# Kernel optimization log

Measured on AMD Instinct MI355X. Metric: run time of the kernel, lower is better.

## Reference

```python
import jax, jax.numpy as jnp
import numpy as np

B, T, C, H = 2, 4096, 512, 8
D = C // H          # head_size = 64
FF = 4 * C          # 2048
EPS = 1e-5


def _layernorm(x, g, b):
    mu = jnp.mean(x, axis=-1, keepdims=True)
    var = jnp.mean(jnp.square(x - mu), axis=-1, keepdims=True)
    return (x - mu) * jax.lax.rsqrt(var + EPS) * g + b


def setup_inputs() -> dict:
    key = jax.random.key(0)
    ks = jax.random.split(key, 10)
    s = 0.02
    return {
        "x":  jax.random.normal(ks[0], (B, T, C), dtype=jnp.float32),
        # per-head K/Q/V linears (bias=False) packed as [C, C] = concat over heads
        "Wq": jax.random.normal(ks[1], (C, C), dtype=jnp.float32) * s,
        "Wk": jax.random.normal(ks[2], (C, C), dtype=jnp.float32) * s,
        "Wv": jax.random.normal(ks[3], (C, C), dtype=jnp.float32) * s,
        "Wo": jax.random.normal(ks[4], (C, C), dtype=jnp.float32) * s,
        "bo": jnp.zeros((C,), dtype=jnp.float32),
        "W1": jax.random.normal(ks[5], (C, FF), dtype=jnp.float32) * s,
        "b1": jnp.zeros((FF,), dtype=jnp.float32),
        "W2": jax.random.normal(ks[6], (FF, C), dtype=jnp.float32) * s,
        "b2": jnp.zeros((C,), dtype=jnp.float32),
        "g1": jnp.ones((C,), dtype=jnp.float32),
        "be1": jnp.zeros((C,), dtype=jnp.float32),
        "g2": jnp.ones((C,), dtype=jnp.float32),
        "be2": jnp.zeros((C,), dtype=jnp.float32),
    }


def reference(x, Wq, Wk, Wv, Wo, bo, W1, b1, W2, b2, g1, be1, g2, be2):
    # --- self-attention on ln1(x), residual add ---
    h = _layernorm(x, g1, be1)                              # [B,T,C]
    q = (h @ Wq).reshape(B, T, H, D)
    k = (h @ Wk).reshape(B, T, H, D)
    v = (h @ Wv).reshape(B, T, H, D)
    # NOTE: original scales by C**-0.5 (n_embd), NOT head_size**-0.5
    scores = jnp.einsum("bthd,bshd->bhts", q, k) * (C ** -0.5)  # [B,H,T,T]
    causal = jnp.tril(jnp.ones((T, T), dtype=bool))
    scores = jnp.where(causal, scores, -jnp.inf)
    wei = jax.nn.softmax(scores, axis=-1)                   # dropout = identity (eval)
    attn = jnp.einsum("bhts,bshd->bthd", wei, v).reshape(B, T, C)
    x = x + (attn @ Wo + bo)                                # proj dropout = identity
    # --- feed-forward on ln2(x), residual add ---
    h2 = _layernorm(x, g2, be2)
    ff = jax.nn.relu(h2 @ W1 + b1) @ W2 + b2                # dropout = identity
    return x + ff
```

## Files before the change

### kernel.cpp

```cpp
#include <hip/hip_runtime.h>

typedef __attribute__((ext_vector_type(8))) __bf16 bf16x8;
typedef __attribute__((ext_vector_type(4))) __bf16 bf16x4;
typedef __attribute__((ext_vector_type(4))) float f32x4;
typedef __attribute__((ext_vector_type(4))) unsigned int u32x4;
typedef __attribute__((ext_vector_type(4))) unsigned short u16x4;
typedef __attribute__((ext_vector_type(8))) unsigned short u16x8;
typedef __attribute__((ext_vector_type(4))) short s16x4;
typedef unsigned short u16;

static __device__ __forceinline__ u16 f2b(float f) {
    unsigned u = __builtin_bit_cast(unsigned, f);
    u = (u + 0x7FFFu + ((u >> 16) & 1u)) >> 16;
    return (u16)u;
}
static __device__ __forceinline__ float b2f(u16 u) {
    return __builtin_bit_cast(float, ((unsigned)u) << 16);
}
static __device__ __forceinline__ float fexp2(float x) {
#if __has_builtin(__builtin_amdgcn_exp2f)
    return __builtin_amdgcn_exp2f(x);
#else
    return exp2f(x);
#endif
}
static __device__ __forceinline__ f32x4 mfma16(bf16x4 a, bf16x4 b, f32x4 c) {
#if __has_builtin(__builtin_amdgcn_mfma_f32_16x16x16_bf16)
    return __builtin_amdgcn_mfma_f32_16x16x16_bf16(a, b, c, 0, 0, 0);
#else
    return __builtin_amdgcn_mfma_f32_16x16x16bf16_1k(
        __builtin_bit_cast(s16x4, a), __builtin_bit_cast(s16x4, b), c, 0, 0, 0);
#endif
}

static __device__ __forceinline__ void gload16(const u16* g, u16* l) {
    __builtin_amdgcn_global_load_lds(
        (const __attribute__((address_space(1))) unsigned int*)g,
        (__attribute__((address_space(3))) unsigned int*)l, 16, 0, 0);
}

__global__ __launch_bounds__(256) void prep_w(
    const float* __restrict__ Wq, const float* __restrict__ Wk,
    const float* __restrict__ Wv, const float* __restrict__ Wo,
    const float* __restrict__ W1, const float* __restrict__ W2,
    u16* __restrict__ WqkvT, u16* __restrict__ WoT,
    u16* __restrict__ W1T, u16* __restrict__ W2T)
{
    const int i = blockIdx.x;
    const float* src; u16* dst; int K, N, nt, kt;
    if (i < 1024) {
        const int z = i >> 8, idx = i & 255;
        K = 512; N = 512; nt = (idx & 15) * 32; kt = (idx >> 4) * 32;
        if (z == 0)      { src = Wq; dst = WqkvT; }
        else if (z == 1) { src = Wk; dst = WqkvT + 512*512; }
        else if (z == 2) { src = Wv; dst = WqkvT + 1024*512; }
        else             { src = Wo; dst = WoT; }
    } else if (i < 2048) {
        const int idx = i - 1024;
        src = W1; dst = W1T; K = 512; N = 2048;
        nt = (idx & 63) * 32; kt = (idx >> 6) * 32;
    } else {
        const int idx = i - 2048;
        src = W2; dst = W2T; K = 2048; N = 512;
        nt = (idx & 15) * 32; kt = (idx >> 4) * 32;
    }
    __shared__ float tile[32][33];
    const int tx = threadIdx.x & 31, ty = threadIdx.x >> 5;
    #pragma unroll
    for (int r = 0; r < 4; ++r)
        tile[ty + r*8][tx] = src[(size_t)(kt + ty + r*8) * N + nt + tx];
    __syncthreads();
    #pragma unroll
    for (int r = 0; r < 4; ++r)
        dst[(size_t)(nt + ty + r*8) * K + kt + tx] = f2b(tile[tx][ty + r*8]);
}

__global__ __launch_bounds__(256) void ln_rows(
    const float* __restrict__ x, const float* __restrict__ g,
    const float* __restrict__ b, u16* __restrict__ out)
{
    const int row = blockIdx.x * 4 + (threadIdx.x >> 6);
    const int lane = threadIdx.x & 63;
    const float* xr = x + (size_t)row * 512;
    f32x4 v0 = *(const f32x4*)(xr + lane * 4);
    f32x4 v1 = *(const f32x4*)(xr + 256 + lane * 4);
    float s = v0[0]+v0[1]+v0[2]+v0[3]+v1[0]+v1[1]+v1[2]+v1[3];
    #pragma unroll
    for (int o = 1; o < 64; o <<= 1) s += __shfl_xor(s, o);
    const float mu = s * (1.0f / 512.0f);
    float s2 = 0.f;
    #pragma unroll
    for (int i = 0; i < 4; ++i) { float d0 = v0[i]-mu, d1 = v1[i]-mu; s2 += d0*d0 + d1*d1; }
    #pragma unroll
    for (int o = 1; o < 64; o <<= 1) s2 += __shfl_xor(s2, o);
    const float inv = rsqrtf(s2 * (1.0f/512.0f) + 1e-5f);
    f32x4 g0 = *(const f32x4*)(g + lane*4), g1 = *(const f32x4*)(g + 256 + lane*4);
    f32x4 b0 = *(const f32x4*)(b + lane*4), b1 = *(const f32x4*)(b + 256 + lane*4);
    u16x4 p0, p1;
    #pragma unroll
    for (int i = 0; i < 4; ++i) {
        p0[i] = f2b((v0[i]-mu)*inv*g0[i] + b0[i]);
        p1[i] = f2b((v1[i]-mu)*inv*g1[i] + b1[i]);
    }
    u16* orow = out + (size_t)row * 512;
    *(u16x4*)(orow + lane*4)       = p0;
    *(u16x4*)(orow + 256 + lane*4) = p1;
}

template<int FLAGS, int NB, int GX>
__global__ __launch_bounds__(256) void gemm_bt(
    const u16* __restrict__ A, const u16* __restrict__ BT,
    const int N, const int K,
    const float* __restrict__ bias, const float* __restrict__ res,
    void* __restrict__ outv, u16* __restrict__ vt)
{
    constexpr int RING = (NB == 2) ? 3 : 4;
    __shared__ __attribute__((aligned(16))) u16 As[RING * 4096];
    __shared__ __attribute__((aligned(16))) u16 Bs[RING * 2048 * NB];
    const int fid = blockIdx.x;
    const int xcd = fid & 7, s8 = fid >> 3;
    const int colb = s8 % GX, rl = s8 / GX;
    const int m0 = (xcd*8 + rl) << 7;
    const int n0 = colb * (64 * NB);
    const int tid = threadIdx.x, lane = tid & 63, w = tid >> 6;
    const int wr2 = w >> 1, wc = w & 1;
    const int g = lane >> 4, c = lane & 15;
    const f32x4 fz = {0.f, 0.f, 0.f, 0.f};

    f32x4 acc[4][2 * NB];
    #pragma unroll
    for (int m = 0; m < 4; ++m)
      #pragma unroll
      for (int n = 0; n < 2 * NB; ++n) acc[m][n] = fz;

    const int srow = tid >> 2;
    const int scs = (((tid & 3) ^ (srow & 3)) * 8);
    const u16* Ag = A  + (size_t)(m0 + srow)*K + scs;
    const u16* Bg = BT + (size_t)(n0 + srow)*K + scs;
    const size_t rstep = (size_t)64 * K;

    const int nkt = K >> 5;
    auto stage = [&](int slot, int kt) {
        const int k0 = kt << 5;
        u16* ad = &As[0] + slot*4096 + w*512;
        gload16(Ag + k0,         ad);
        gload16(Ag + rstep + k0, ad + 2048);
        u16* bd = &Bs[0] + slot*2048*NB + w*512;
        gload16(Bg + k0, bd);
        if constexpr (NB == 2) gload16(Bg + rstep + k0, bd + 2048);
    };
    stage(0, 0);
    stage(1, (1 < nkt) ? 1 : 0);
    if constexpr (RING == 4) stage(2, (2 < nkt) ? 2 : 0);

    for (int kt = 0; kt < nkt; ++kt) {
        if constexpr (NB == 2) asm volatile("s_waitcnt vmcnt(4)" ::: "memory");
        else                   asm volatile("s_waitcnt vmcnt(6)" ::: "memory");
        __builtin_amdgcn_s_barrier();
        asm volatile("" ::: "memory");
        {
            int tp = kt + RING - 1; if (tp >= nkt) tp = nkt - 1;
            int sl = kt + RING - 1; sl -= (sl / RING) * RING;
            stage(sl, tp);
        }
        const int rd = kt - (kt / RING) * RING;
        const u16* Ab = &As[0] + rd*4096;
        const u16* Bb = &Bs[0] + rd*2048*NB;
        bf16x8 af[4], bfr[2 * NB];
        #pragma unroll
        for (int m = 0; m < 4; ++m) {
            const int row = wr2*64 + m*16 + c;
            af[m] = *(const bf16x8*)(Ab + row*32 + (((g*16) ^ ((row&3)<<4)) >> 1));
        }
        #pragma unroll
        for (int n = 0; n < 2 * NB; ++n) {
            const int row = wc*(32*NB) + n*16 + c;
            bfr[n] = *(const bf16x8*)(Bb + row*32 + (((g*16) ^ ((row&3)<<4)) >> 1));
        }
        #pragma unroll
        for (int m = 0; m < 4; ++m)
          #pragma unroll
          for (int n = 0; n < 2 * NB; ++n)
            acc[m][n] = __builtin_amdgcn_mfma_f32_16x16x32_bf16(af[m], bfr[n], acc[m][n], 0, 0, 0);
    }

    #pragma unroll
    for (int m = 0; m < 4; ++m) {
        const int row = m0 + wr2*64 + m*16 + 4*g;
        #pragma unroll
        for (int n = 0; n < 2 * NB; ++n) {
            const int col = n0 + wc*(32*NB) + n*16 + c;
            const float bv = (FLAGS & 1) ? bias[col] : 0.0f;
            float vv[4];
            #pragma unroll
            for (int r = 0; r < 4; ++r) {
                float v = acc[m][n][r] + bv;
                if (FLAGS & 16) v *= (col < 512) ? 0.0637587246f : 1.0f;
                if (FLAGS & 2) v += res[(size_t)(row + r)*N + col];
                if (FLAGS & 4) v = fmaxf(v, 0.0f);
                vv[r] = v;
            }
            if ((FLAGS & 32) && col >= 1024) {
                u16x4 pv;
                #pragma unroll
                for (int r = 0; r < 4; ++r) pv[r] = f2b(vv[r]);
                *(u16x4*)(vt + (size_t)((row >> 12)*512 + (col - 1024))*4096
                             + (row & 4095)) = pv;
            } else if (FLAGS & 8) {
                #pragma unroll
                for (int r = 0; r < 4; ++r)
                    ((float*)outv)[(size_t)(row + r)*N + col] = vv[r];
            } else {
                #pragma unroll
                for (int r = 0; r < 4; ++r)
                    ((u16*)outv)[(size_t)(row + r)*N + col] = f2b(vv[r]);
            }
        }
    }
}

template<int FLAGS, int GX>
__global__ __launch_bounds__(256) void gemm_m64(
    const u16* __restrict__ A, const u16* __restrict__ BT,
    const int N, const int K,
    const float* __restrict__ bias, const float* __restrict__ res,
    void* __restrict__ outv)
{
    __shared__ __attribute__((aligned(16))) u16 As[4 * 2048];
    __shared__ __attribute__((aligned(16))) u16 Bs[4 * 2048];
    const int fid = blockIdx.x;
    const int xcd = fid & 7, s8 = fid >> 3;
    const int colb = s8 % GX, rl = s8 / GX;
    const int m0 = (xcd*16 + rl) << 6;
    const int n0 = colb << 6;
    const int tid = threadIdx.x, lane = tid & 63, w = tid >> 6;
    const int g = lane >> 4, c = lane & 15;
    const f32x4 fz = {0.f, 0.f, 0.f, 0.f};

    f32x4 acc[4] = {fz, fz, fz, fz};

    const int srow = tid >> 2;
    const int scs = (((tid & 3) ^ (srow & 3)) * 8);
    const u16* Ag = A  + (size_t)(m0 + srow)*K + scs;
    const u16* Bg = BT + (size_t)(n0 + srow)*K + scs;

    const int nkt = K >> 5;
    auto stage = [&](int slot, int kt) {
        const int k0 = kt << 5;
        gload16(Ag + k0, &As[0] + slot*2048 + w*512);
        gload16(Bg + k0, &Bs[0] + slot*2048 + w*512);
    };
    stage(0, 0);
    stage(1, (1 < nkt) ? 1 : 0);
    stage(2, (2 < nkt) ? 2 : 0);

    const int arow = w*16 + c;
    const int aoff = arow*32 + ((g ^ (arow & 3)) * 8);
    for (int kt = 0; kt < nkt; ++kt) {
        asm volatile("s_waitcnt vmcnt(4)" ::: "memory");
        __builtin_amdgcn_s_barrier();
        asm volatile("" ::: "memory");
        {
            int tp = kt + 3; if (tp >= nkt) tp = nkt - 1;
            stage((kt + 3) & 3, tp);
        }
        const int rd = kt & 3;
        const u16* Ab = &As[0] + rd*2048;
        const u16* Bb = &Bs[0] + rd*2048;
        const bf16x8 af = *(const bf16x8*)(Ab + aoff);
        bf16x8 bfr[4];
        #pragma unroll
        for (int n = 0; n < 4; ++n) {
            const int row = n*16 + c;
            bfr[n] = *(const bf16x8*)(Bb + row*32 + ((g ^ (row & 3)) * 8));
        }
        #pragma unroll
        for (int n = 0; n < 4; ++n)
            acc[n] = __builtin_amdgcn_mfma_f32_16x16x32_bf16(af, bfr[n], acc[n], 0, 0, 0);
    }

    const int row = m0 + w*16 + 4*g;
    #pragma unroll
    for (int n = 0; n < 4; ++n) {
        const int col = n0 + n*16 + c;
        const float bv = (FLAGS & 1) ? bias[col] : 0.0f;
        #pragma unroll
        for (int r = 0; r < 4; ++r) {
            float v = acc[n][r] + bv;
            if (FLAGS & 2) v += res[(size_t)(row + r)*N + col];
            if (FLAGS & 4) v = fmaxf(v, 0.0f);
            if (FLAGS & 8) ((float*)outv)[(size_t)(row + r)*N + col] = v;
            else           ((u16*)outv)[(size_t)(row + r)*N + col] = f2b(v);
        }
    }
}

__global__ __launch_bounds__(256, 3) void attn_fwd(
    const u16* __restrict__ qkv, const u16* __restrict__ vT,
    u16* __restrict__ part, u16* __restrict__ att)
{
    const int fid = blockIdx.x + 160 * blockIdx.y;
    const int xcd = fid & 7, s0i = fid >> 3;
    const int half = (s0i >= 160) ? 1 : 0;
    const int bh = xcd*2 + half, b = bh >> 3, h = bh & 7;
    const int i = 159 - (s0i - half*160);
    int qt, cch, nch;
    if (i < 16)      { qt = i;                         cch = 0;          nch = 1; }
    else if (i < 48) { int j = i-16; qt = 16 + (j>>1); cch = j & 1;      nch = 2; }
    else if (i < 96) { int j = i-48; int d3 = j/3; qt = 32 + d3; cch = j - 3*d3; nch = 3; }
    else             { int j = i-96; qt = 48 + (j>>2); cch = j & 3;      nch = 4; }
    const int ntl = qt + 1;
    const int t0 = (cch * ntl) / nch;
    const int t1 = ((cch + 1) * ntl) / nch;
    const int single = (nch == 1);

    const int tid = threadIdx.x, lane = tid & 63, w = tid >> 6;
    const int g = lane >> 4, c16 = lane & 15;
    __shared__ __attribute__((aligned(16))) u16 smem[20480];
    u16* Wb = smem + w*5120;
    float* lbuf = (float*)smem + 5120;

    const u16* qp  = qkv + (size_t)b*4096*1536 + h*64;
    const u16* kp  = qp + 512;
    const u16* vtp = vT + (size_t)bh*64*4096;

    const u16* kgA = kp + (size_t)(16*w + (lane>>3))*1536
                        + (((lane&7) ^ ((lane>>3)&7)) * 8);
    const u16* kgB = kgA + (size_t)8*1536;
    const int sd = lane >> 1;
    const u16* vgA = vtp + (size_t)sd*4096 + 16*w + (((lane&1) ^ ((sd>>2)&1)) * 8);
    const u16* vgB = vgA + (size_t)32*4096;

    const int kOff0 = c16*64 + ((g ^ (c16&7)) * 8);
    const int kOff1 = c16*64 + (((4+g) ^ (c16&7)) * 8);
    const int vroff = c16*16 + (((g>>1) ^ ((c16>>2)&1)) * 8) + (g&1)*4;

    const int Q0 = qt*64;
    bf16x8 qB[4][2];
    #pragma unroll
    for (int sub = 0; sub < 4; ++sub) {
        const u16* qr = qp + (size_t)(Q0 + sub*16 + c16)*1536 + g*8;
        qB[sub][0] = *(const bf16x8*)(qr);
        qB[sub][1] = *(const bf16x8*)(qr + 32);
    }

    const f32x4 fz = {0.f,0.f,0.f,0.f};
    f32x4 oacc[4][4];
    #pragma unroll
    for (int dt = 0; dt < 4; ++dt)
      #pragma unroll
      for (int sub = 0; sub < 4; ++sub) oacc[dt][sub] = fz;
    float lsum[4] = {0.f, 0.f, 0.f, 0.f};

    {
        const int kv0 = t0 << 6;
        u16* vd = Wb + 3072 + (t0 & 1)*1024;
        gload16(vgA + kv0, vd); gload16(vgB + kv0, vd + 512);
        u16* kd = Wb + (t0 % 3)*1024;
        const size_t ko0 = (size_t)kv0 * 1536;
        gload16(kgA + ko0, kd); gload16(kgB + ko0, kd + 512);
        const int tp1 = (t0+1 < t1) ? (t0+1) : (t1-1);
        u16* kd1 = Wb + ((t0+1) % 3)*1024;
        const size_t ko1 = (size_t)(tp1 << 6)*1536;
        gload16(kgA + ko1, kd1); gload16(kgB + ko1, kd1 + 512);
    }
    int krd = t0 % 3;
    int kwr = krd + 2; if (kwr >= 3) kwr -= 3;

    for (int t = t0; t < t1; ++t) {
        {
            const int tpv = (t+1 < t1) ? (t+1) : (t1-1);
            u16* vd = Wb + 3072 + ((t+1) & 1)*1024;
            gload16(vgA + (tpv << 6), vd); gload16(vgB + (tpv << 6), vd + 512);
            const int tpk = (t+2 < t1) ? (t+2) : (t1-1);
            u16* kd = Wb + kwr*1024;
            const size_t ko = (size_t)(tpk << 6)*1536;
            gload16(kgA + ko, kd); gload16(kgB + ko, kd + 512);
        }
        asm volatile("s_waitcnt vmcnt(6)" ::: "memory");
        const u16* Kb  = Wb + krd*1024;
        const u16* Vbp = Wb + 3072 + (t & 1)*1024;
        const bf16x8 kc0 = *(const bf16x8*)(Kb + kOff0);
        const bf16x8 kc1 = *(const bf16x8*)(Kb + kOff1);
        bf16x4 va[4];
        #pragma unroll
        for (int dt = 0; dt < 4; ++dt)
            va[dt] = *(const bf16x4*)(Vbp + dt*256 + vroff);
        f32x4 s[4];
        #pragma unroll
        for (int sub = 0; sub < 4; ++sub) {
            f32x4 sv = __builtin_amdgcn_mfma_f32_16x16x32_bf16(kc0, qB[sub][0], fz, 0, 0, 0);
            s[sub]   = __builtin_amdgcn_mfma_f32_16x16x32_bf16(kc1, qB[sub][1], sv, 0, 0, 0);
        }
        bf16x4 pt[4];
        if (t < qt) {
            #pragma unroll
            for (int sub = 0; sub < 4; ++sub) {
                float p0 = fexp2(s[sub][0]), p1 = fexp2(s[sub][1]);
                float p2 = fexp2(s[sub][2]), p3 = fexp2(s[sub][3]);
                lsum[sub] += (p0 + p1) + (p2 + p3);
                bf16x4 pv;
                pv[0] = (__bf16)p0; pv[1] = (__bf16)p1;
                pv[2] = (__bf16)p2; pv[3] = (__bf16)p3;
                pt[sub] = pv;
            }
        } else {
            const int kvbase = t*64 + 16*w + 4*g;
            #pragma unroll
            for (int sub = 0; sub < 4; ++sub) {
                const int qi = Q0 + sub*16 + c16;
                bf16x4 pv; float a = 0.f;
                #pragma unroll
                for (int r = 0; r < 4; ++r) {
                    float p = (kvbase + r <= qi) ? fexp2(s[sub][r]) : 0.0f;
                    a += p; pv[r] = (__bf16)p;
                }
                lsum[sub] += a; pt[sub] = pv;
            }
        }
        #pragma unroll
        for (int dt = 0; dt < 4; ++dt)
          #pragma unroll
          for (int sub = 0; sub < 4; ++sub)
            oacc[dt][sub] = mfma16(va[dt], pt[sub], oacc[dt][sub]);
        krd = (krd == 2) ? 0 : krd + 1;
        kwr = (kwr == 2) ? 0 : kwr + 1;
    }

    #pragma unroll
    for (int sub = 0; sub < 4; ++sub) {
        float v = lsum[sub];
        v += __shfl_xor(v, 16);
        v += __shfl_xor(v, 32);
        lsum[sub] = v;
    }

    asm volatile("s_waitcnt vmcnt(0)" ::: "memory");
    __syncthreads();
    #pragma unroll
    for (int sub = 0; sub < 4; ++sub)
        if (g == 0) lbuf[w*64 + sub*16 + c16] = lsum[sub];

    float* img = (float*)smem;
    f32x4 ofin[4];
    float ltot[4];
    #pragma unroll
    for (int dt = 0; dt < 4; ++dt) {
        #pragma unroll
        for (int sub = 0; sub < 4; ++sub)
            *(f32x4*)(img + w*1280 + (sub*16 + c16)*20 + g*4) = oacc[dt][sub];
        __syncthreads();
        if (dt == 0) {
            #pragma unroll
            for (int sub = 0; sub < 4; ++sub) {
                const int qr = sub*16 + c16;
                ltot[sub] = lbuf[qr] + lbuf[64 + qr] + lbuf[128 + qr] + lbuf[192 + qr];
            }
        }
        if (w == dt) {
            #pragma unroll
            for (int sub = 0; sub < 4; ++sub) {
                const int off = (sub*16 + c16)*20 + g*4;
                f32x4 a0 = *(const f32x4*)(img + off);
                f32x4 a1 = *(const f32x4*)(img + 1280 + off);
                f32x4 a2 = *(const f32x4*)(img + 2560 + off);
                f32x4 a3 = *(const f32x4*)(img + 3840 + off);
                ofin[sub] = (a0 + a1) + (a2 + a3);
            }
        }
        __syncthreads();
    }

    const int dbase = 16*w + 4*g;
    if (single) {
        #pragma unroll
        for (int sub = 0; sub < 4; ++sub) {
            const int qrow = sub*16 + c16;
            const float inv = 1.0f / ltot[sub];
            const f32x4 o = ofin[sub];
            u16x4 ov;
            ov[0] = f2b(o[0]*inv); ov[1] = f2b(o[1]*inv);
            ov[2] = f2b(o[2]*inv); ov[3] = f2b(o[3]*inv);
            *(u16x4*)(att + (size_t)(b*4096 + Q0 + qrow)*512 + h*64 + dbase) = ov;
        }
    } else {
        u16* onum = part + (size_t)(bh*160 + i) * 4224;
        float* lout = (float*)(onum + 4096);
        #pragma unroll
        for (int sub = 0; sub < 4; ++sub) {
            const int qrow = sub*16 + c16;
            const f32x4 o = ofin[sub];
            u16x4 ov;
            ov[0] = f2b(o[0]); ov[1] = f2b(o[1]);
            ov[2] = f2b(o[2]); ov[3] = f2b(o[3]);
            *(u16x4*)(onum + qrow*64 + dbase) = ov;
            if (w == 0 && g == 0) lout[qrow] = ltot[sub];
        }
    }
}

__global__ __launch_bounds__(256) void attn_merge(
    const u16* __restrict__ part, u16* __restrict__ att)
{
    const int qt = 16 + blockIdx.x, bh = blockIdx.y, b = bh >> 3, h = bh & 7;
    int start, n;
    if (qt < 32)      { start = 16 + 2*(qt-16); n = 2; }
    else if (qt < 48) { start = 48 + 3*(qt-32); n = 3; }
    else              { start = 96 + 4*(qt-48); n = 4; }
    const int t = threadIdx.x;
    const int row = t >> 2, c0 = (t & 3) * 16;
    float acc[16];
    #pragma unroll
    for (int j = 0; j < 16; ++j) acc[j] = 0.f;
    float lt = 0.f;
    const u16* p0 = part + (size_t)(bh*160 + start) * 4224;
    for (int ci = 0; ci < n; ++ci) {
        const u16* pc = p0 + (size_t)ci * 4224;
        lt += ((const float*)(pc + 4096))[row];
        u16x8 a = *(const u16x8*)(pc + row*64 + c0);
        u16x8 bq = *(const u16x8*)(pc + row*64 + c0 + 8);
        #pragma unroll
        for (int j = 0; j < 8; ++j) { acc[j] += b2f(a[j]); acc[8+j] += b2f(bq[j]); }
    }
    const float inv = 1.0f / lt;
    u16x8 o1, o2;
    #pragma unroll
    for (int j = 0; j < 8; ++j) { o1[j] = f2b(acc[j]*inv); o2[j] = f2b(acc[8+j]*inv); }
    u16* dst = att + (size_t)(b*4096 + qt*64 + row)*512 + h*64 + c0;
    *(u16x8*)dst = o1;
    *(u16x8*)(dst + 8) = o2;
}

extern "C" void kernel_launch(void* const* d_in, const int* in_sizes, int n_in,
                              void* d_out, int out_size, void* d_ws, size_t ws_size,
                              hipStream_t stream)
{
    (void)in_sizes; (void)n_in; (void)out_size; (void)ws_size;
    const float* x   = (const float*)d_in[0];
    const float* Wq  = (const float*)d_in[1];
    const float* Wk  = (const float*)d_in[2];
    const float* Wv  = (const float*)d_in[3];
    const float* Wo  = (const float*)d_in[4];
    const float* bo  = (const float*)d_in[5];
    const float* W1  = (const float*)d_in[6];
    const float* b1  = (const float*)d_in[7];
    const float* W2  = (const float*)d_in[8];
    const float* b2  = (const float*)d_in[9];
    const float* g1  = (const float*)d_in[10];
    const float* be1 = (const float*)d_in[11];
    const float* g2  = (const float*)d_in[12];
    const float* be2 = (const float*)d_in[13];

    char* ws = (char*)d_ws;
    u16*   WqkvT = (u16*)(ws + 0);
    u16*   WoT   = (u16*)(ws + 1572864);
    u16*   W1T   = (u16*)(ws + 2097152);
    u16*   W2T   = (u16*)(ws + 4194304);
    u16*   H     = (u16*)(ws + 6291456);
    u16*   PART  = (u16*)(ws + 6291456);
    float* X2    = (float*)(ws + 14680064);
    u16*   QKV   = (u16*)(ws + 31457280);
    u16*   VT    = (u16*)(ws + 56623104);
    u16*   ATT   = (u16*)(ws + 65011712);
    u16*   F1    = (u16*)(ws + 31457280);

    prep_w<<<3072, 256, 0, stream>>>(Wq, Wk, Wv, Wo, W1, W2,
                                     WqkvT, WoT, W1T, W2T);
    ln_rows<<<2048, 256, 0, stream>>>(x, g1, be1, H);
    gemm_bt<48, 2, 12><<<768, 256, 0, stream>>>(H, WqkvT, 1536, 512,
                                                nullptr, nullptr, QKV, VT);
    attn_fwd<<<dim3(160, 16), 256, 0, stream>>>(QKV, VT, PART, ATT);
    attn_merge<<<dim3(48, 16), 256, 0, stream>>>(PART, ATT);
    gemm_m64<11, 8><<<1024, 256, 0, stream>>>(ATT, WoT, 512, 512,
                                              bo, x, X2);
    ln_rows<<<2048, 256, 0, stream>>>(X2, g2, be2, H);
    gemm_bt<5, 2, 16><<<1024, 256, 0, stream>>>(H, W1T, 2048, 512,
                                                b1, nullptr, F1, nullptr);
    gemm_m64<11, 8><<<1024, 256, 0, stream>>>(F1, W2T, 512, 2048,
                                              b2, X2, (float*)d_out);
}
```

Baseline: 189.6 us.

## Stage Q tile in LDS and shrink K prefetch to double buffering

Q fragments are no longer held in registers for the whole loop. The Q tile is loaded once into swizzled shared memory and reread by every wave each iteration. The K ring buffer shrinks from triple to double buffering, so K prefetch now runs one tile ahead instead of two and the wait count drops from 6 to 4. This lowers VGPR pressure and the per-wave LDS footprint, trading for extra LDS reads per iteration and less latency hiding on K loads.

Measured after the change: 187.8 us, median of 2. No clear change (-1.0%).

```diff
diff --git a/kernel.cpp b/kernel.cpp
--- a/kernel.cpp
+++ b/kernel.cpp
@@ -317,7 +317,8 @@
     const int tid = threadIdx.x, lane = tid & 63, w = tid >> 6;
     const int g = lane >> 4, c16 = lane & 15;
     __shared__ __attribute__((aligned(16))) u16 smem[20480];
-    u16* Wb = smem + w*5120;
+    u16* Wb = smem + w*4096;
+    u16* Qs = smem + 16384;
     float* lbuf = (float*)smem + 5120;
 
     const u16* qp  = qkv + (size_t)b*4096*1536 + h*64;
@@ -336,13 +337,16 @@
     const int vroff = c16*16 + (((g>>1) ^ ((c16>>2)&1)) * 8) + (g&1)*4;
 
     const int Q0 = qt*64;
-    bf16x8 qB[4][2];
-    #pragma unroll
-    for (int sub = 0; sub < 4; ++sub) {
-        const u16* qr = qp + (size_t)(Q0 + sub*16 + c16)*1536 + g*8;
-        qB[sub][0] = *(const bf16x8*)(qr);
-        qB[sub][1] = *(const bf16x8*)(qr + 32);
-    }
+    {
+        const int qrow = tid >> 2;
+        const int ch0 = (tid & 3) * 2, ch1 = ch0 + 1;
+        const u16* qsrc = qp + (size_t)(Q0 + qrow)*1536 + ch0*8;
+        u16x8 d0 = *(const u16x8*)(qsrc);
+        u16x8 d1 = *(const u16x8*)(qsrc + 8);
+        *(u16x8*)(Qs + qrow*64 + ((ch0 ^ (qrow&7))*8)) = d0;
+        *(u16x8*)(Qs + qrow*64 + ((ch1 ^ (qrow&7))*8)) = d1;
+    }
+    __syncthreads();
 
     const f32x4 fz = {0.f,0.f,0.f,0.f};
     f32x4 oacc[4][4];
@@ -354,32 +358,26 @@
 
     {
         const int kv0 = t0 << 6;
-        u16* vd = Wb + 3072 + (t0 & 1)*1024;
+        u16* vd = Wb + 2048 + (t0 & 1)*1024;
         gload16(vgA + kv0, vd); gload16(vgB + kv0, vd + 512);
-        u16* kd = Wb + (t0 % 3)*1024;
+        u16* kd = Wb + (t0 & 1)*1024;
         const size_t ko0 = (size_t)kv0 * 1536;
         gload16(kgA + ko0, kd); gload16(kgB + ko0, kd + 512);
-        const int tp1 = (t0+1 < t1) ? (t0+1) : (t1-1);
-        u16* kd1 = Wb + ((t0+1) % 3)*1024;
-        const size_t ko1 = (size_t)(tp1 << 6)*1536;
-        gload16(kgA + ko1, kd1); gload16(kgB + ko1, kd1 + 512);
-    }
-    int krd = t0 % 3;
-    int kwr = krd + 2; if (kwr >= 3) kwr -= 3;
+    }
 
     for (int t = t0; t < t1; ++t) {
         {
-            const int tpv = (t+1 < t1) ? (t+1) : (t1-1);
-            u16* vd = Wb + 3072 + ((t+1) & 1)*1024;
-            gload16(vgA + (tpv << 6), vd); gload16(vgB + (tpv << 6), vd + 512);
-            const int tpk = (t+2 < t1) ? (t+2) : (t1-1);
-            u16* kd = Wb + kwr*1024;
-            const size_t ko = (size_t)(tpk << 6)*1536;
+            const int tp = (t+1 < t1) ? (t+1) : (t1-1);
+            const int kv = tp << 6;
+            u16* vd = Wb + 2048 + ((t+1) & 1)*1024;
+            gload16(vgA + kv, vd); gload16(vgB + kv, vd + 512);
+            u16* kd = Wb + ((t+1) & 1)*1024;
+            const size_t ko = (size_t)kv * 1536;
             gload16(kgA + ko, kd); gload16(kgB + ko, kd + 512);
         }
-        asm volatile("s_waitcnt vmcnt(6)" ::: "memory");
-        const u16* Kb  = Wb + krd*1024;
-        const u16* Vbp = Wb + 3072 + (t & 1)*1024;
+        asm volatile("s_waitcnt vmcnt(4)" ::: "memory");
+        const u16* Kb  = Wb + (t & 1)*1024;
+        const u16* Vbp = Wb + 2048 + (t & 1)*1024;
         const bf16x8 kc0 = *(const bf16x8*)(Kb + kOff0);
         const bf16x8 kc1 = *(const bf16x8*)(Kb + kOff1);
         bf16x4 va[4];
@@ -389,8 +387,11 @@
         f32x4 s[4];
         #pragma unroll
         for (int sub = 0; sub < 4; ++sub) {
-            f32x4 sv = __builtin_amdgcn_mfma_f32_16x16x32_bf16(kc0, qB[sub][0], fz, 0, 0, 0);
-            s[sub]   = __builtin_amdgcn_mfma_f32_16x16x32_bf16(kc1, qB[sub][1], sv, 0, 0, 0);
+            const int qrow = sub*16 + c16;
+            const bf16x8 qb0 = *(const bf16x8*)(Qs + qrow*64 + ((g ^ (c16&7))*8));
+            const bf16x8 qb1 = *(const bf16x8*)(Qs + qrow*64 + (((4+g) ^ (c16&7))*8));
+            f32x4 sv = __builtin_amdgcn_mfma_f32_16x16x32_bf16(kc0, qb0, fz, 0, 0, 0);
+            s[sub]   = __builtin_amdgcn_mfma_f32_16x16x32_bf16(kc1, qb1, sv, 0, 0, 0);
         }
         bf16x4 pt[4];
         if (t < qt) {
@@ -423,8 +424,6 @@
           #pragma unroll
           for (int sub = 0; sub < 4; ++sub)
             oacc[dt][sub] = mfma16(va[dt], pt[sub], oacc[dt][sub]);
-        krd = (krd == 2) ? 0 : krd + 1;
-        kwr = (kwr == 2) ? 0 : kwr + 1;
     }
 
     #pragma unroll
```
